# Optimization experiments

Hardware: AMD Instinct MI355X
Metric: run time of the kernel (lower is better)

## Reference

```python
import jax, jax.numpy as jnp
import numpy as np

NEW_AMP = 0.2
THRESHOLD = 0.5
B, N, F = 512, 2048, 16


def setup_inputs() -> dict:
    key = jax.random.key(0)
    k1, k2 = jax.random.split(key)
    data = jax.random.normal(k1, (B, N), dtype=jnp.float32)
    filt = jax.random.uniform(k2, (F,), dtype=jnp.float32)  # matched-filter template
    return {"data": data, "filt": filt}


def reference(data, filt):
    # Faithful translation of MHSA.mhsa_encode.
    # f = filter * new_amp (the torch module scales self.filter in place once per call)
    f = filt * jnp.asarray(NEW_AMP, dtype=filt.dtype)  # [F]
    n = data.shape[1]
    Fs = f.shape[0]

    def encode_row(row):  # row: [N]
        def step(row, i):
            # fits == (i + F - 1 < N) == (i + F <= N): same condition guards both
            # the error accumulation and the subtractive update in the original.
            fits = (i + Fs) <= n
            # dynamic_slice clamps the start index, safe for tail i (never written back then)
            win = jax.lax.dynamic_slice(row, (i,), (Fs,))

            def body(j, carry):
                err, win, out = carry
                d = win[j]
                # error += filter[j] - data[i+j]  when data[i+j] < filter[j] and window fits
                err = err + jnp.where(jnp.logical_and(fits, d < f[j]), f[j] - d, jnp.float32(0.0))
                # checked INSIDE the j loop in the original: output set and window
                # decremented by the whole filter each j while error <= threshold
                cond = err <= THRESHOLD
                out = jnp.logical_or(out, cond)
                win = jnp.where(jnp.logical_and(cond, fits), win - f, win)
                return (err, win, out)

            err, win, out = jax.lax.fori_loop(
                0, Fs, body, (jnp.float32(0.0), win, jnp.bool_(False))
            )
            row = jnp.where(fits, jax.lax.dynamic_update_slice(row, win, (i,)), row)
            return row, out.astype(jnp.float32)

        _, outs = jax.lax.scan(step, row, jnp.arange(n))
        return outs  # [N] of 0/1 floats

    return jax.vmap(encode_row)(data)  # [B, N]
```

## Files before the change

### kernel.cpp

```cpp
#include <hip/hip_runtime.h>


constexpr int NN = 2048;
constexpr int NBLK = 512;

__device__ __forceinline__ float f_readlane(float v, int lane) {
    return __int_as_float(__builtin_amdgcn_readlane(__float_as_int(v), lane));
}

__device__ __forceinline__ float f_slide(float src, float fill) {
    return __int_as_float(__builtin_amdgcn_update_dpp(
        __float_as_int(fill), __float_as_int(src),
        0x101 , 0xF, 0xF, false));
}

__global__ __launch_bounds__(64) void mhsa_kernel(const float* __restrict__ data,
                                                  const float* __restrict__ filt,
                                                  float* __restrict__ out) {
    __shared__ float lrow[NN];
    const int row = blockIdx.x;
    const int tid = threadIdx.x;
    const int j = tid & 15;

    const float* rp = data + (size_t)row * NN;
    float* op = out + (size_t)row * NN;

    const float4* rp4 = (const float4*)rp;
    float4* l4 = (float4*)lrow;
#pragma unroll
    for (int k = 0; k < NN / 4 / 64; ++k)
        l4[tid + 64 * k] = rp4[tid + 64 * k];
    __syncthreads();

    const float fv = filt[j] * 0.2f;
    float v = lrow[j];

    for (int ib = 0; ib < NN - 16; ib += 16) {
        unsigned obits = 0;
#pragma unroll
        for (int s = 0; s < 16; ++s) {
            const float nxt = lrow[ib + 16 + s];

            float t = fmaxf(fv - v, 0.0f);
            float err = f_readlane(t, 0);
            if (err <= 0.5f) {
                obits |= (1u << s);
#pragma unroll
                for (int r = 1; r <= 16; ++r) {
                    v = v - fv;
                    if (r == 16) break;
                    float tr = fmaxf(fv - v, 0.0f);
                    err += f_readlane(tr, r);
                    if (!(err <= 0.5f)) break;
                }
            }
            v = f_slide(v, nxt);
        }
        op[ib + j] = ((obits >> j) & 1u) ? 1.0f : 0.0f;
    }

    {
        float t = fmaxf(fv - v, 0.0f);
        float err = f_readlane(t, 0);
        float v0 = (err <= 0.5f) ? 1.0f : 0.0f;
        op[(NN - 16) + j] = (j == 0) ? v0 : 1.0f;
    }
}

extern "C" void kernel_launch(void* const* d_in, const int* in_sizes, int n_in,
                              void* d_out, int out_size, void* d_ws, size_t ws_size,
                              hipStream_t stream) {
    const float* data = (const float*)d_in[0];
    const float* filt = (const float*)d_in[1];
    float* out = (float*)d_out;
    (void)in_sizes; (void)n_in; (void)out_size; (void)d_ws; (void)ws_size;
    mhsa_kernel<<<dim3(NBLK), dim3(64), 0, stream>>>(data, filt, out);
}
```

Before: 188.7 us.

## Speculate first four filter taps branch-free and prefetch next LDS chunk into registers

Replaces the serial per-tap readlane/branch chain with a speculative computation of the first four subtractive steps, whose cumulative errors are evaluated together and applied through selects. A rolled loop is entered only when all four taps pass. It also prefetches the next 16 samples from LDS as float4 registers one block ahead, with zero padding past the row end. The aim is to shorten the dependent scalar/branch latency chain and hide LDS load latency. The cost is extra ALU work and readlanes on every step, plus higher register pressure.

New measurement: 296.9 us. 1.57x slower.

```diff
diff --git a/kernel.cpp b/kernel.cpp
--- a/kernel.cpp
+++ b/kernel.cpp
@@ -17,7 +17,7 @@
 __global__ __launch_bounds__(64) void mhsa_kernel(const float* __restrict__ data,
                                                   const float* __restrict__ filt,
                                                   float* __restrict__ out) {
-    __shared__ float lrow[NN];
+    __shared__ float lrow[NN + 32];
     const int row = blockIdx.x;
     const int tid = threadIdx.x;
     const int j = tid & 15;
@@ -30,39 +30,69 @@
 #pragma unroll
     for (int k = 0; k < NN / 4 / 64; ++k)
         l4[tid + 64 * k] = rp4[tid + 64 * k];
+    if (tid < 8) l4[NN / 4 + tid] = make_float4(0.f, 0.f, 0.f, 0.f);
     __syncthreads();
 
     const float fv = filt[j] * 0.2f;
     float v = lrow[j];
 
+    float4 n0 = l4[4], n1 = l4[5], n2 = l4[6], n3 = l4[7];
+
     for (int ib = 0; ib < NN - 16; ib += 16) {
+        const float4* pf = (const float4*)(lrow + ib + 32);
+        float4 p0 = pf[0], p1 = pf[1], p2 = pf[2], p3 = pf[3];
+
         unsigned obits = 0;
 #pragma unroll
         for (int s = 0; s < 16; ++s) {
-            const float nxt = lrow[ib + 16 + s];
+            const float4 q = (s < 4) ? n0 : (s < 8) ? n1 : (s < 12) ? n2 : n3;
+            const int c = s & 3;
+            const float nxt = (c == 0) ? q.x : (c == 1) ? q.y
+                            : (c == 2) ? q.z : q.w;
 
-            float t = fmaxf(fv - v, 0.0f);
-            float err = f_readlane(t, 0);
-            if (err <= 0.5f) {
-                obits |= (1u << s);
-#pragma unroll
-                for (int r = 1; r <= 16; ++r) {
+            float w1 = v - fv;
+            float w2 = w1 - fv;
+            float w3 = w2 - fv;
+            float t0 = fmaxf(fv - v, 0.0f);
+            float t1 = fmaxf(fv - w1, 0.0f);
+            float t2 = fmaxf(fv - w2, 0.0f);
+            float t3 = fmaxf(fv - w3, 0.0f);
+            float e0 = f_readlane(t0, 0);
+            float e1 = e0 + f_readlane(t1, 1);
+            float e2 = e1 + f_readlane(t2, 2);
+            float e3 = e2 + f_readlane(t3, 3);
+            const bool k1 = (e0 <= 0.5f);
+            const bool k2 = (e1 <= 0.5f);
+            const bool k3 = (e2 <= 0.5f);
+            if (k1) obits |= (1u << s);
+
+            if (e3 <= 0.5f) {
+                v = w3;
+                float err = e3;
+#pragma unroll 1
+                for (int r = 4; r <= 16; ++r) {
                     v = v - fv;
                     if (r == 16) break;
                     float tr = fmaxf(fv - v, 0.0f);
                     err += f_readlane(tr, r);
                     if (!(err <= 0.5f)) break;
                 }
+            } else {
+                v = k1 ? w1 : v;
+                v = k2 ? w2 : v;
+                v = k3 ? w3 : v;
             }
             v = f_slide(v, nxt);
         }
         op[ib + j] = ((obits >> j) & 1u) ? 1.0f : 0.0f;
+
+        n0 = p0; n1 = p1; n2 = p2; n3 = p3;
     }
 
     {
-        float t = fmaxf(fv - v, 0.0f);
-        float err = f_readlane(t, 0);
-        float v0 = (err <= 0.5f) ? 1.0f : 0.0f;
+        float t0 = fmaxf(fv - v, 0.0f);
+        float e0 = f_readlane(t0, 0);
+        float v0 = (e0 <= 0.5f) ? 1.0f : 0.0f;
         op[(NN - 16) + j] = (j == 0) ? v0 : 1.0f;
     }
 }
```
